# Optimization experiments

Measured on AMD Instinct MI355X. Metric: run time of the kernel, lower is better.

Reference implementation:

```python
import jax, jax.numpy as jnp
import numpy as np
import math

DIM = 384
NUM_HEADS = 12
WS = 8  # window_size


def setup_inputs() -> dict:
    key = jax.random.key(0)
    k1, k2, k3 = jax.random.split(key, 3)
    B, N, C = 16, 4096, DIM
    x = jax.random.normal(k1, (B, N, C), dtype=jnp.float32)
    W_qkv = jax.random.normal(k2, (C, 3 * C), dtype=jnp.float32) * 0.02
    b_qkv = jnp.zeros((3 * C,), dtype=jnp.float32)
    W_proj = jax.random.normal(k3, (C, C), dtype=jnp.float32) * 0.02
    return {"x": x, "W_qkv": W_qkv, "b_qkv": b_qkv, "W_proj": W_proj}


def window_attention(x, W_qkv, b_qkv, W_proj):
    B, N, C = x.shape
    H = W = int(math.isqrt(N))
    nh = NUM_HEADS
    hd = C // nh
    scale = hd ** (-0.5)
    ws = WS
    pad_h = (ws - H % ws) % ws
    pad_w = (ws - W % ws) % ws
    xg = x.reshape(B, H, W, C)
    if pad_h or pad_w:
        xg = jnp.pad(xg, ((0, 0), (0, pad_h), (0, pad_w), (0, 0)))
    Hp, Wp = H + pad_h, W + pad_w
    nH, nW = Hp // ws, Wp // ws
    # partition into windows: [B, nWin, ws*ws, C]
    xw = xg.reshape(B, nH, ws, nW, ws, C).transpose(0, 1, 3, 2, 4, 5)
    xw = xw.reshape(B, nH * nW, ws * ws, C)
    # qkv projection
    qkv = xw @ W_qkv + b_qkv  # [B, nWin, ws2, 3C]
    qkv = qkv.reshape(B, nH * nW, ws * ws, 3, nh, hd)
    q = qkv[..., 0, :, :].transpose(0, 1, 3, 2, 4)  # [B, nWin, nh, ws2, hd]
    k = qkv[..., 1, :, :].transpose(0, 1, 3, 2, 4)
    v = qkv[..., 2, :, :].transpose(0, 1, 3, 2, 4)
    attn = jnp.einsum('bwhqd,bwhkd->bwhqk', q, k) * scale
    attn = jax.nn.softmax(attn, axis=-1)
    out = jnp.einsum('bwhqk,bwhkd->bwhqd', attn, v)
    out = out.transpose(0, 1, 3, 2, 4).reshape(B, nH * nW, ws * ws, C)
    out = out @ W_proj
    # un-partition windows
    out = out.reshape(B, nH, nW, ws, ws, C).transpose(0, 1, 3, 2, 4, 5)
    out = out.reshape(B, Hp, Wp, C)
    if pad_h or pad_w:
        out = out[:, :H, :W, :]
    return out.reshape(B, H * W, C)


def reference(x, W_qkv, b_qkv, W_proj):
    return window_attention(x, W_qkv, b_qkv, W_proj)
```

## Files before the change

### kernel.cpp

```cpp
#include <hip/hip_runtime.h>
#include <hip/hip_bf16.h>


typedef _Float16 f16;
typedef f16 f16x8 __attribute__((ext_vector_type(8)));
typedef f16 f16x4 __attribute__((ext_vector_type(4)));
typedef float f32x4 __attribute__((ext_vector_type(4)));

#define MFMA_F16(a, b, c) __builtin_amdgcn_mfma_f32_16x16x32_f16((a), (b), (c), 0, 0, 0)

#define AS_G __attribute__((address_space(1)))
#define AS_L __attribute__((address_space(3)))
#define GLOAD_LDS16(gp, lp) \
  __builtin_amdgcn_global_load_lds((const AS_G void*)(gp), (AS_L void*)(lp), 16, 0, 0)
#define WAITVM_(N) asm volatile("s_waitcnt vmcnt(" #N ")" ::: "memory")
#define WAITVM(N) WAITVM_(N)

namespace {
constexpr int kC = 384;
constexpr int kNTok = 4096;
constexpr float kScale = 0.17677669529663687f;
constexpr int kWqPackChunks = 72 * 12 * 64;
constexpr int kWpPackChunks = 24 * 12 * 64;
constexpr size_t kWqPackBytes = (size_t)kWqPackChunks * 16;
constexpr size_t kWpPackBytes = (size_t)kWpPackChunks * 16;
constexpr size_t kQkvWsBytes = (size_t)65536 * 1152 * 2;
constexpr size_t kWsNeed = kWqPackBytes + kWpPackBytes + kQkvWsBytes;
constexpr int kPrepXBlocks = 12288;
constexpr int kQkvPackChunksFb = 6 * 12 * 12 * 64;
}


__global__ void prep_all(const float* __restrict__ x,
                         const float* __restrict__ Wqkv,
                         const float* __restrict__ Wproj,
                         f16* __restrict__ xw, f16* __restrict__ wq_pack,
                         f16* __restrict__ wp_pack) {
  int blk = blockIdx.x;
  if (blk < kPrepXBlocks) {
    int c = blk * 256 + threadIdx.x;
    int lane = c & 63;
    int t = c >> 6;
    int ks = t % 12;
    int mb = t / 12;
    int l15 = lane & 15, g = lane >> 4;
    int m = mb * 16 + l15;
    int b = m >> 12;
    int win = (m >> 6) & 63;
    int tok = m & 63;
    int n = ((win >> 3) * 8 + (tok >> 3)) * 64 + (win & 7) * 8 + (tok & 7);
    const float* src = x + ((size_t)(b << 12) + n) * kC + ks * 32 + g * 8;
    float4 v0 = *reinterpret_cast<const float4*>(src);
    float4 v1 = *reinterpret_cast<const float4*>(src + 4);
    f16x8 h = {(f16)v0.x, (f16)v0.y, (f16)v0.z, (f16)v0.w,
               (f16)v1.x, (f16)v1.y, (f16)v1.z, (f16)v1.w};
    *reinterpret_cast<f16x8*>(xw + (size_t)c * 8) = h;
    return;
  }
  int i = (blk - kPrepXBlocks) * 256 + threadIdx.x;
  if (i < kWqPackChunks) {
    int lane = i & 63;
    int chunk = i >> 6;
    int ks = chunk % 12;
    int t = chunk / 12;
    int l15 = lane & 15, g = lane >> 4;
    int n3 = t * 16 + l15;
    int k0 = ks * 32 + g * 8;
    f16x8 v;
    #pragma unroll
    for (int j = 0; j < 8; ++j)
      v[j] = (f16)Wqkv[(size_t)(k0 + j) * (3 * kC) + n3];
    *reinterpret_cast<f16x8*>(wq_pack + (size_t)i * 8) = v;
  } else if (i < kWqPackChunks + kWpPackChunks) {
    int p = i - kWqPackChunks;
    int lane = p & 63;
    int chunk = p >> 6;
    int ks = chunk % 12;
    int t = chunk / 12;
    int l15 = lane & 15, g = lane >> 4;
    int n = t * 16 + l15;
    int k0 = ks * 32 + g * 8;
    f16x8 v;
    #pragma unroll
    for (int j = 0; j < 8; ++j)
      v[j] = (f16)Wproj[(size_t)(k0 + j) * kC + n];
    *reinterpret_cast<f16x8*>(wp_pack + (size_t)p * 8) = v;
  }
}

__global__ __launch_bounds__(512, 4) void qkv_gemm6(
    const f16* __restrict__ xw, const float* __restrict__ b_qkv,
    const f16* __restrict__ wq_pack, f16* __restrict__ qkv_ws) {
  __shared__ alignas(1024) char smem[73728];

  const int tid = threadIdx.x;
  const int wid = tid >> 6;
  const int lane = tid & 63;
  const int g = lane >> 4;
  const int l15 = lane & 15;
  const int wm = wid >> 1;
  const int wn = wid & 1;

  int bid = blockIdx.x;
  int wg = (bid & 7) * 288 + (bid >> 3);
  int m_grp = wg / 9;
  int n_grp = wg - m_grp * 9;
  const int mb0 = m_grp * 16;
  const int nb0 = n_grp * 8;

  #define STAGE(KS, BUF)                                                       \
    do {                                                                       \
      const f16* ga0 =                                                         \
          xw + (((size_t)(mb0 + wid) * 12 + (KS)) * 64 + lane) * 8;            \
      const f16* ga1 =                                                         \
          xw + (((size_t)(mb0 + 8 + wid) * 12 + (KS)) * 64 + lane) * 8;        \
      const f16* gb0 =                                                         \
          wq_pack + (((size_t)(nb0 + wid) * 12 + (KS)) * 64 + lane) * 8;       \
      char* la = smem + (BUF) * 24576 + wid * 1024;                            \
      char* lb = smem + (BUF) * 24576 + 16384 + wid * 1024;                    \
      GLOAD_LDS16(ga0, la);                                                    \
      GLOAD_LDS16(ga1, la + 8192);                                             \
      GLOAD_LDS16(gb0, lb);                                                    \
    } while (0)

  f32x4 acc[4][4];
  #pragma unroll
  for (int mt = 0; mt < 4; ++mt)
    #pragma unroll
    for (int nt = 0; nt < 4; ++nt) acc[mt][nt] = {0.f, 0.f, 0.f, 0.f};

  STAGE(0, 0);
  STAGE(1, 1);
  STAGE(2, 2);
  WAITVM(6);
  __builtin_amdgcn_sched_barrier(0);
  __builtin_amdgcn_s_barrier();

  #define KITER(T, ENDVM)                                                      \
    do {                                                                       \
      constexpr int buf = (T) % 3;                                             \
      f16x8 af[4], bf[4];                                                      \
      _Pragma("unroll") for (int mt = 0; mt < 4; ++mt) af[mt] =                \
          *reinterpret_cast<const f16x8*>(smem + buf * 24576 +                 \
                                          (wm * 4 + mt) * 1024 + lane * 16);   \
      _Pragma("unroll") for (int nt = 0; nt < 4; ++nt) bf[nt] =                \
          *reinterpret_cast<const f16x8*>(smem + buf * 24576 + 16384 +         \
                                          (wn * 4 + nt) * 1024 + lane * 16);   \
      asm volatile("s_waitcnt lgkmcnt(0)" ::: "memory");                       \
      __builtin_amdgcn_sched_barrier(0);                                       \
      __builtin_amdgcn_s_barrier();                                            \
      if ((T) < 9) {                                                           \
        STAGE((T) + 3, buf);                                                   \
      }                                                                        \
      __builtin_amdgcn_s_setprio(1);                                           \
      _Pragma("unroll") for (int mt = 0; mt < 4; ++mt)                         \
          _Pragma("unroll") for (int nt = 0; nt < 4; ++nt) acc[mt][nt] =       \
          MFMA_F16(af[mt], bf[nt], acc[mt][nt]);                               \
      __builtin_amdgcn_s_setprio(0);                                           \
      WAITVM(ENDVM);                                                           \
      __builtin_amdgcn_sched_barrier(0);                                       \
      __builtin_amdgcn_s_barrier();                                            \
    } while (0)

  KITER(0, 6);
  KITER(1, 6);
  KITER(2, 6);
  KITER(3, 6);
  KITER(4, 6);
  KITER(5, 6);
  KITER(6, 6);
  KITER(7, 6);
  KITER(8, 6);
  KITER(9, 3);
  KITER(10, 0);
  KITER(11, 0);
  #undef KITER
  #undef STAGE

  f16* eo = (f16*)smem;
  #pragma unroll
  for (int nt = 0; nt < 4; ++nt) {
    int col128 = wn * 64 + nt * 16 + l15;
    float bias = b_qkv[n_grp * 128 + col128];
    int hsec_loc = wn * 2 + (nt >> 1);
    int d = col128 & 31;
    int sec = (n_grp * 4 + hsec_loc) / 12;
    int base = (wm * 4 + hsec_loc) * 2048;
    #pragma unroll
    for (int mt = 0; mt < 4; ++mt) {
      #pragma unroll
      for (int j = 0; j < 4; ++j) {
        int tok = mt * 16 + g * 4 + j;
        f16 hv = (f16)(acc[mt][nt][j] + bias);
        if (sec == 2)
          eo[base + d * 64 + (tok ^ ((d & 7) << 3))] = hv;
        else
          eo[base + tok * 32 + d] = hv;
      }
    }
  }
  __syncthreads();
  #pragma unroll
  for (int i = 0; i < 8; ++i) {
    int u = tid + i * 512;
    int win_loc = u >> 10;
    int cbl = (u >> 8) & 3;
    int inner = u & 255;
    int cb = n_grp * 4 + cbl;
    int h = cb % 12;
    int sec = cb / 12;
    size_t dst = ((size_t)(m_grp * 4 + win_loc) * 36 + h * 3 + sec) * 2048 +
                 (size_t)inner * 8;
    f16x8 hv;
    if (sec == 2) {
      int d = inner >> 3;
      int t0 = inner & 7;
      hv = *reinterpret_cast<const f16x8*>(eo + (win_loc * 4 + cbl) * 2048 +
                                           d * 64 + ((t0 * 8) ^ ((d & 7) << 3)));
    } else {
      hv = *reinterpret_cast<const f16x8*>(eo + (size_t)u * 8);
    }
    *reinterpret_cast<f16x8*>(qkv_ws + dst) = hv;
  }
}

__device__ __forceinline__ void load_qkv(const f16* __restrict__ hb,
                                         f16x8 (&qf)[4], f16x8 (&kf)[4],
                                         f16x8 (&vf)[2][2], int g, int l15) {
  #pragma unroll
  for (int mt = 0; mt < 4; ++mt)
    qf[mt] = *reinterpret_cast<const f16x8*>(hb + (mt * 16 + l15) * 32 + g * 8);
  #pragma unroll
  for (int nt = 0; nt < 4; ++nt)
    kf[nt] = *reinterpret_cast<const f16x8*>(hb + 2048 + (nt * 16 + l15) * 32 +
                                             g * 8);
  #pragma unroll
  for (int nd = 0; nd < 2; ++nd)
    #pragma unroll
    for (int ks = 0; ks < 2; ++ks)
      vf[nd][ks] = *reinterpret_cast<const f16x8*>(
          hb + 4096 + (nd * 16 + l15) * 64 + ks * 32 + g * 8);
}

__device__ __forceinline__ void attn_one(const f16x8 (&qf)[4],
                                         const f16x8 (&kf)[4],
                                         const f16x8 (&vf)[2][2],
                                         f16 (&ao)[64][392], f16 (&ps)[16][68],
                                         int wid, int g, int l15) {
  const f32x4 zero4 = {0.f, 0.f, 0.f, 0.f};
  #pragma unroll
  for (int mt = 0; mt < 4; ++mt) {
    f32x4 sw0 = MFMA_F16(kf[0], qf[mt], zero4);
    f32x4 sw1 = MFMA_F16(kf[1], qf[mt], zero4);
    f32x4 sw2 = MFMA_F16(kf[2], qf[mt], zero4);
    f32x4 sw3 = MFMA_F16(kf[3], qf[mt], zero4);
    float p[16];
    #pragma unroll
    for (int j = 0; j < 4; ++j) {
      p[j] = sw0[j] * kScale;
      p[4 + j] = sw1[j] * kScale;
      p[8 + j] = sw2[j] * kScale;
      p[12 + j] = sw3[j] * kScale;
    }
    float m0 = fmaxf(fmaxf(p[0], p[1]), fmaxf(p[2], p[3]));
    float m1 = fmaxf(fmaxf(p[4], p[5]), fmaxf(p[6], p[7]));
    float m2 = fmaxf(fmaxf(p[8], p[9]), fmaxf(p[10], p[11]));
    float m3 = fmaxf(fmaxf(p[12], p[13]), fmaxf(p[14], p[15]));
    float mx = fmaxf(fmaxf(m0, m1), fmaxf(m2, m3));
    mx = fmaxf(mx, __shfl_xor(mx, 16));
    mx = fmaxf(mx, __shfl_xor(mx, 32));
    #pragma unroll
    for (int i = 0; i < 16; ++i) p[i] = __expf(p[i] - mx);
    float s01 = (p[0] + p[1]) + (p[2] + p[3]);
    float s23 = (p[4] + p[5]) + (p[6] + p[7]);
    float s45 = (p[8] + p[9]) + (p[10] + p[11]);
    float s67 = (p[12] + p[13]) + (p[14] + p[15]);
    float s = (s01 + s23) + (s45 + s67);
    s += __shfl_xor(s, 16);
    s += __shfl_xor(s, 32);
    float inv = __builtin_amdgcn_rcpf(s);
    #pragma unroll
    for (int nt = 0; nt < 4; ++nt) {
      f16x4 h = {(f16)(p[nt * 4] * inv), (f16)(p[nt * 4 + 1] * inv),
                 (f16)(p[nt * 4 + 2] * inv), (f16)(p[nt * 4 + 3] * inv)};
      *reinterpret_cast<f16x4*>(&ps[l15][nt * 16 + g * 4]) = h;
    }
    f32x4 o0 = zero4, o1 = zero4;
    #pragma unroll
    for (int ks = 0; ks < 2; ++ks) {
      f16x8 pa = *reinterpret_cast<const f16x8*>(&ps[l15][ks * 32 + g * 8]);
      o0 = MFMA_F16(pa, vf[0][ks], o0);
      o1 = MFMA_F16(pa, vf[1][ks], o1);
    }
    #pragma unroll
    for (int j = 0; j < 4; ++j) {
      ao[mt * 16 + g * 4 + j][wid * 32 + l15] = (f16)o0[j];
      ao[mt * 16 + g * 4 + j][wid * 32 + 16 + l15] = (f16)o1[j];
    }
  }
}

__device__ __forceinline__ void proj_store(const f16 (&ao)[64][392],
                                           const f16* __restrict__ wp_pack,
                                           float* __restrict__ out, int b,
                                           int win, int wid, int g, int l15,
                                           int lane) {
  const f32x4 zero4 = {0.f, 0.f, 0.f, 0.f};
  const int wh = win >> 3, ww = win & 7;
  f32x4 pacc[4][2];
  #pragma unroll
  for (int mt = 0; mt < 4; ++mt) {
    pacc[mt][0] = zero4;
    pacc[mt][1] = zero4;
  }
  const f16* pp0 = wp_pack + ((size_t)((wid * 2) * 12) * 64 + lane) * 8;
  const f16* pp1 = wp_pack + ((size_t)((wid * 2 + 1) * 12) * 64 + lane) * 8;
  f16x8 pb0[2], pb1[2];
  pb0[0] = *reinterpret_cast<const f16x8*>(pp0);
  pb1[0] = *reinterpret_cast<const f16x8*>(pp1);
  #pragma unroll
  for (int ks = 0; ks < 12; ++ks) {
    const int cur = ks & 1;
    if (ks < 11) {
      pb0[cur ^ 1] = *reinterpret_cast<const f16x8*>(pp0 + (ks + 1) * 512);
      pb1[cur ^ 1] = *reinterpret_cast<const f16x8*>(pp1 + (ks + 1) * 512);
    }
    f16x8 paf[4];
    #pragma unroll
    for (int mt = 0; mt < 4; ++mt)
      paf[mt] = *reinterpret_cast<const f16x8*>(
          &ao[mt * 16 + l15][ks * 32 + g * 8]);
    #pragma unroll
    for (int mt = 0; mt < 4; ++mt) {
      pacc[mt][0] = MFMA_F16(paf[mt], pb0[cur], pacc[mt][0]);
      pacc[mt][1] = MFMA_F16(paf[mt], pb1[cur], pacc[mt][1]);
    }
  }
  const size_t outbase = (size_t)b * kNTok * kC;
  #pragma unroll
  for (int mt = 0; mt < 4; ++mt) {
    #pragma unroll
    for (int j = 0; j < 4; ++j) {
      int rr = mt * 16 + g * 4 + j;
      int n = (wh * 8 + (rr >> 3)) * 64 + ww * 8 + (rr & 7);
      float* orow = out + outbase + (size_t)n * kC + wid * 32;
      orow[l15] = pacc[mt][0][j];
      orow[16 + l15] = pacc[mt][1][j];
    }
  }
}

__global__ __launch_bounds__(768, 3) void attn_proj3(
    const f16* __restrict__ qkv_ws, const f16* __restrict__ wp_pack,
    float* __restrict__ out) {
  __shared__ alignas(16) f16 ao[64][392];
  __shared__ alignas(16) f16 p_s[12][16][68];

  const int tid = threadIdx.x;
  const int wid = tid >> 6;
  const int lane = tid & 63;
  const int g = lane >> 4;
  const int l15 = lane & 15;

  int bid = (int)blockIdx.x;
  int w2 = (bid & 7) * 64 + (bid >> 3);
  const int b = w2 >> 5;
  const int win0 = (w2 & 31) * 2;
  const int win1 = win0 + 1;

  const f16* hb0 = qkv_ws + ((size_t)(b * 64 + win0) * 36 + wid * 3) * 2048;
  const f16* hb1 = hb0 + 36 * 2048;

  f16x8 qA[4], kA[4], vA[2][2], qB[4], kB[4], vB[2][2];
  load_qkv(hb0, qA, kA, vA, g, l15);
  __builtin_amdgcn_sched_barrier(0);
  attn_one(qA, kA, vA, ao, p_s[wid], wid, g, l15);
  load_qkv(hb1, qB, kB, vB, g, l15);
  __builtin_amdgcn_sched_barrier(0);
  __syncthreads();
  proj_store(ao, wp_pack, out, b, win0, wid, g, l15, lane);
  __syncthreads();
  attn_one(qB, kB, vB, ao, p_s[wid], wid, g, l15);
  __syncthreads();
  proj_store(ao, wp_pack, out, b, win1, wid, g, l15, lane);
}


__global__ void prep_weights_fb(const float* __restrict__ Wqkv,
                                const float* __restrict__ Wproj,
                                f16* __restrict__ wq_pack,
                                f16* __restrict__ wp_pack) {
  int i = blockIdx.x * 256 + threadIdx.x;
  if (i < kQkvPackChunksFb) {
    int lane = i & 63;
    int chunk = i >> 6;
    int ks = chunk % 12;
    int t = (chunk / 12) % 12;
    int hp = chunk / 144;
    int l15 = lane & 15, g = lane >> 4;
    int base = t * 16;
    int hh = base / 96;
    int cc = base - hh * 96;
    int sec = cc >> 5;
    int dbhi = cc & 31;
    int n3 = sec * kC + (2 * hp + hh) * 32 + dbhi + l15;
    int k0 = ks * 32 + g * 8;
    f16x8 v;
    #pragma unroll
    for (int j = 0; j < 8; ++j)
      v[j] = (f16)Wqkv[(size_t)(k0 + j) * (3 * kC) + n3];
    *reinterpret_cast<f16x8*>(wq_pack + (size_t)i * 8) = v;
  } else if (i < kQkvPackChunksFb + kWpPackChunks) {
    int p = i - kQkvPackChunksFb;
    int lane = p & 63;
    int chunk = p >> 6;
    int ks = chunk % 12;
    int t = chunk / 12;
    int l15 = lane & 15, g = lane >> 4;
    int n = t * 16 + l15;
    int k0 = ks * 32 + g * 8;
    f16x8 v;
    #pragma unroll
    for (int j = 0; j < 8; ++j)
      v[j] = (f16)Wproj[(size_t)(k0 + j) * kC + n];
    *reinterpret_cast<f16x8*>(wp_pack + (size_t)p * 8) = v;
  }
}

__global__ __launch_bounds__(512, 2) void win_attn_fused_fb(
    const float* __restrict__ x, const float* __restrict__ b_qkv,
    const f16* __restrict__ wq_pack, const f16* __restrict__ wp_pack,
    float* __restrict__ out) {
  __shared__ alignas(16) f16 xs[64][392];
  __shared__ alignas(16) f16 ao[64][392];
  __shared__ alignas(16) f16 q_s[2][64][40];
  __shared__ alignas(16) f16 k_s[2][64][40];
  __shared__ alignas(16) f16 vT[2][32][72];
  __shared__ alignas(16) f16 p_s[8][16][72];

  const int tid = threadIdx.x;
  const int wid = tid >> 6;
  const int lane = tid & 63;
  const int g = lane >> 4;
  const int l15 = lane & 15;
  const int wm = wid >> 2;
  const int wn = wid & 3;

  const int blk = blockIdx.x;
  const int b = blk >> 6;
  const int win = blk & 63;
  const int wh = win >> 3;
  const int ww = win & 7;

  const f32x4 zero4 = {0.f, 0.f, 0.f, 0.f};

  {
    const float* xb = x + (size_t)b * kNTok * kC;
    #pragma unroll
    for (int it = 0; it < 12; ++it) {
      int idx = tid + it * 512;
      int r = idx / 96;
      int c4 = idx - r * 96;
      int n = (wh * 8 + (r >> 3)) * 64 + ww * 8 + (r & 7);
      float4 v = *reinterpret_cast<const float4*>(xb + (size_t)n * kC + c4 * 4);
      f16x4 hv = {(f16)v.x, (f16)v.y, (f16)v.z, (f16)v.w};
      *reinterpret_cast<f16x4*>(&xs[r][c4 * 4]) = hv;
    }
  }
  __syncthreads();

  for (int hp = 0; hp < 6; ++hp) {
    f32x4 acc[2][3];
    #pragma unroll
    for (int mt = 0; mt < 2; ++mt)
      #pragma unroll
      for (int nt = 0; nt < 3; ++nt) acc[mt][nt] = zero4;

    const f16* bptr[3];
    int secv[3], dbv[3], hhv[3];
    #pragma unroll
    for (int nt = 0; nt < 3; ++nt) {
      int t = wn * 3 + nt;
      int base = t * 16;
      int hh = base / 96;
      int cc = base - hh * 96;
      hhv[nt] = hh;
      secv[nt] = cc >> 5;
      dbv[nt] = cc & 31;
      bptr[nt] = wq_pack + ((size_t)((hp * 12 + t) * 12) * 64 + lane) * 8;
    }

    f16x8 bf[4][3];
    f16x8 af[2][2];
    #pragma unroll
    for (int p = 0; p < 3; ++p)
      #pragma unroll
      for (int nt = 0; nt < 3; ++nt)
        bf[p][nt] = *reinterpret_cast<const f16x8*>(bptr[nt] + p * 512);
    #pragma unroll
    for (int mt = 0; mt < 2; ++mt)
      af[0][mt] = *reinterpret_cast<const f16x8*>(
          &xs[wm * 32 + mt * 16 + l15][g * 8]);

    #pragma unroll
    for (int ks = 0; ks < 12; ++ks) {
      const int cur = ks & 3;
      const int ca = ks & 1;
      if (ks < 9) {
        const int nx = (ks + 3) & 3;
        #pragma unroll
        for (int nt = 0; nt < 3; ++nt)
          bf[nx][nt] =
              *reinterpret_cast<const f16x8*>(bptr[nt] + (ks + 3) * 512);
      }
      if (ks < 11) {
        #pragma unroll
        for (int mt = 0; mt < 2; ++mt)
          af[ca ^ 1][mt] = *reinterpret_cast<const f16x8*>(
              &xs[wm * 32 + mt * 16 + l15][(ks + 1) * 32 + g * 8]);
      }
      #pragma unroll
      for (int mt = 0; mt < 2; ++mt)
        #pragma unroll
        for (int nt = 0; nt < 3; ++nt)
          acc[mt][nt] = MFMA_F16(af[ca][mt], bf[cur][nt], acc[mt][nt]);
    }

    #pragma unroll
    for (int nt = 0; nt < 3; ++nt) {
      int hh = hhv[nt], sec = secv[nt];
      int col = dbv[nt] + l15;
      float bias = b_qkv[sec * kC + (2 * hp + hh) * 32 + col];
      #pragma unroll
      for (int mt = 0; mt < 2; ++mt) {
        #pragma unroll
        for (int j = 0; j < 4; ++j) {
          int r = wm * 32 + mt * 16 + g * 4 + j;
          f16 hv = (f16)(acc[mt][nt][j] + bias);
          if (sec == 0) q_s[hh][r][col] = hv;
          else if (sec == 1) k_s[hh][r][col] = hv;
          else vT[hh][col][r] = hv;
        }
      }
    }
    __syncthreads();

    f32x4 sacc[4];
    #pragma unroll
    for (int nt = 0; nt < 4; ++nt) sacc[nt] = zero4;
    f16x8 qa = *reinterpret_cast<const f16x8*>(&q_s[wm][wn * 16 + l15][g * 8]);
    #pragma unroll
    for (int nt = 0; nt < 4; ++nt) {
      f16x8 kb =
          *reinterpret_cast<const f16x8*>(&k_s[wm][nt * 16 + l15][g * 8]);
      sacc[nt] = MFMA_F16(qa, kb, sacc[nt]);
    }

    float pv[4][4];
    #pragma unroll
    for (int j = 0; j < 4; ++j) {
      float m = -1e30f;
      #pragma unroll
      for (int nt = 0; nt < 4; ++nt) {
        pv[nt][j] = sacc[nt][j] * kScale;
        m = fmaxf(m, pv[nt][j]);
      }
      m = fmaxf(m, __shfl_xor(m, 1));
      m = fmaxf(m, __shfl_xor(m, 2));
      m = fmaxf(m, __shfl_xor(m, 4));
      m = fmaxf(m, __shfl_xor(m, 8));
      float s = 0.f;
      #pragma unroll
      for (int nt = 0; nt < 4; ++nt) {
        pv[nt][j] = __expf(pv[nt][j] - m);
        s += pv[nt][j];
      }
      s += __shfl_xor(s, 1);
      s += __shfl_xor(s, 2);
      s += __shfl_xor(s, 4);
      s += __shfl_xor(s, 8);
      float inv = 1.0f / s;
      #pragma unroll
      for (int nt = 0; nt < 4; ++nt)
        p_s[wid][g * 4 + j][nt * 16 + l15] = (f16)(pv[nt][j] * inv);
    }

    f32x4 oacc[2];
    oacc[0] = zero4;
    oacc[1] = zero4;
    #pragma unroll
    for (int ks = 0; ks < 2; ++ks) {
      f16x8 pa =
          *reinterpret_cast<const f16x8*>(&p_s[wid][l15][ks * 32 + g * 8]);
      #pragma unroll
      for (int nt = 0; nt < 2; ++nt) {
        f16x8 vb = *reinterpret_cast<const f16x8*>(
            &vT[wm][nt * 16 + l15][ks * 32 + g * 8]);
        oacc[nt] = MFMA_F16(pa, vb, oacc[nt]);
      }
    }
    #pragma unroll
    for (int nt = 0; nt < 2; ++nt)
      #pragma unroll
      for (int j = 0; j < 4; ++j)
        ao[wn * 16 + g * 4 + j][(2 * hp + wm) * 32 + nt * 16 + l15] =
            (f16)oacc[nt][j];
    __syncthreads();
  }

  f32x4 pacc[2][6];
  #pragma unroll
  for (int mt = 0; mt < 2; ++mt)
    #pragma unroll
    for (int nt = 0; nt < 6; ++nt) pacc[mt][nt] = zero4;

  const f16* pptr[6];
  #pragma unroll
  for (int nt = 0; nt < 6; ++nt) {
    int t = wn * 6 + nt;
    pptr[nt] = wp_pack + ((size_t)(t * 12) * 64 + lane) * 8;
  }
  f16x8 pbf[3][6];
  f16x8 paf[2][2];
  #pragma unroll
  for (int p = 0; p < 2; ++p)
    #pragma unroll
    for (int nt = 0; nt < 6; ++nt)
      pbf[p][nt] = *reinterpret_cast<const f16x8*>(pptr[nt] + p * 512);
  #pragma unroll
  for (int mt = 0; mt < 2; ++mt)
    paf[0][mt] =
        *reinterpret_cast<const f16x8*>(&ao[wm * 32 + mt * 16 + l15][g * 8]);

  #pragma unroll
  for (int ks = 0; ks < 12; ++ks) {
    const int cur = ks % 3;
    const int ca = ks & 1;
    if (ks < 10) {
      const int nx = (ks + 2) % 3;
      #pragma unroll
      for (int nt = 0; nt < 6; ++nt)
        pbf[nx][nt] =
            *reinterpret_cast<const f16x8*>(pptr[nt] + (ks + 2) * 512);
    }
    if (ks < 11) {
      #pragma unroll
      for (int mt = 0; mt < 2; ++mt)
        paf[ca ^ 1][mt] = *reinterpret_cast<const f16x8*>(
            &ao[wm * 32 + mt * 16 + l15][(ks + 1) * 32 + g * 8]);
    }
    #pragma unroll
    for (int mt = 0; mt < 2; ++mt)
      #pragma unroll
      for (int nt = 0; nt < 6; ++nt)
        pacc[mt][nt] = MFMA_F16(paf[ca][mt], pbf[cur][nt], pacc[mt][nt]);
  }

  const size_t outbase = (size_t)b * kNTok * kC;
  #pragma unroll
  for (int mt = 0; mt < 2; ++mt) {
    #pragma unroll
    for (int j = 0; j < 4; ++j) {
      int r = wm * 32 + mt * 16 + g * 4 + j;
      int n = (wh * 8 + (r >> 3)) * 64 + ww * 8 + (r & 7);
      float* orow = out + outbase + (size_t)n * kC + wn * 96;
      #pragma unroll
      for (int nt = 0; nt < 6; ++nt) orow[nt * 16 + l15] = pacc[mt][nt][j];
    }
  }
}


extern "C" void kernel_launch(void* const* d_in, const int* in_sizes, int n_in,
                              void* d_out, int out_size, void* d_ws,
                              size_t ws_size, hipStream_t stream) {
  const float* x = (const float*)d_in[0];
  const float* Wqkv = (const float*)d_in[1];
  const float* bqkv = (const float*)d_in[2];
  const float* Wproj = (const float*)d_in[3];
  float* out = (float*)d_out;

  if (ws_size >= kWsNeed) {
    f16* wq_pack = (f16*)d_ws;
    f16* wp_pack = (f16*)((char*)d_ws + kWqPackBytes);
    f16* qkv_ws = (f16*)((char*)d_ws + kWqPackBytes + kWpPackBytes);
    f16* xw = (f16*)d_out;

    int prep_blocks =
        kPrepXBlocks + (kWqPackChunks + kWpPackChunks + 255) / 256;
    hipLaunchKernelGGL(prep_all, dim3(prep_blocks), dim3(256), 0, stream, x,
                       Wqkv, Wproj, xw, wq_pack, wp_pack);
    hipLaunchKernelGGL(qkv_gemm6, dim3(2304), dim3(512), 0, stream, xw, bqkv,
                       wq_pack, qkv_ws);
    hipLaunchKernelGGL(attn_proj3, dim3(512), dim3(768), 0, stream, qkv_ws,
                       wp_pack, out);
  } else {
    f16* wq_pack = (f16*)d_ws;
    f16* wp_pack = (f16*)((char*)d_ws + (size_t)kQkvPackChunksFb * 16);
    int prep_threads = kQkvPackChunksFb + kWpPackChunks;
    hipLaunchKernelGGL(prep_weights_fb, dim3((prep_threads + 255) / 256),
                       dim3(256), 0, stream, Wqkv, Wproj, wq_pack, wp_pack);
    hipLaunchKernelGGL(win_attn_fused_fb, dim3(16 * 64), dim3(512), 0, stream,
                       x, bqkv, wq_pack, wp_pack, out);
  }
}
```

Measured before the change: 160.8 us.

## Use four larger-tile warps per block in QKV GEMM instead of eight

Cuts the QKV GEMM block from 8 to 4 wavefronts while keeping the same 256x128 output tile. Each wave now computes a 64x128 sub-tile (4x8 MFMA tiles) and reuses the A fragments across twice as many B fragments, which lowers LDS reads per MFMA. Each thread issues 6 async global-to-LDS loads per stage, and the vmcnt waits are scaled to match. The trade-off is more accumulator registers per thread and fewer waves per block available to hide latency.

```diff
diff --git a/kernel.cpp b/kernel.cpp
--- a/kernel.cpp
+++ b/kernel.cpp
@@ -88,7 +88,7 @@
   }
 }
 
-__global__ __launch_bounds__(512, 4) void qkv_gemm6(
+__global__ __launch_bounds__(256, 2) void qkv_gemm8(
     const f16* __restrict__ xw, const float* __restrict__ b_qkv,
     const f16* __restrict__ wq_pack, f16* __restrict__ qkv_ws) {
   __shared__ alignas(1024) char smem[73728];
@@ -98,8 +98,6 @@
   const int lane = tid & 63;
   const int g = lane >> 4;
   const int l15 = lane & 15;
-  const int wm = wid >> 1;
-  const int wn = wid & 1;
 
   int bid = blockIdx.x;
   int wg = (bid & 7) * 288 + (bid >> 3);
@@ -110,42 +108,43 @@
 
   #define STAGE(KS, BUF)                                                       \
     do {                                                                       \
-      const f16* ga0 =                                                         \
-          xw + (((size_t)(mb0 + wid) * 12 + (KS)) * 64 + lane) * 8;            \
-      const f16* ga1 =                                                         \
-          xw + (((size_t)(mb0 + 8 + wid) * 12 + (KS)) * 64 + lane) * 8;        \
-      const f16* gb0 =                                                         \
-          wq_pack + (((size_t)(nb0 + wid) * 12 + (KS)) * 64 + lane) * 8;       \
-      char* la = smem + (BUF) * 24576 + wid * 1024;                            \
-      char* lb = smem + (BUF) * 24576 + 16384 + wid * 1024;                    \
-      GLOAD_LDS16(ga0, la);                                                    \
-      GLOAD_LDS16(ga1, la + 8192);                                             \
-      GLOAD_LDS16(gb0, lb);                                                    \
+      char* la = smem + (BUF) * 24576;                                         \
+      char* lb = la + 16384;                                                   \
+      _Pragma("unroll") for (int q = 0; q < 4; ++q) {                          \
+        const f16* ga =                                                        \
+            xw + (((size_t)(mb0 + wid + q * 4) * 12 + (KS)) * 64 + lane) * 8;  \
+        GLOAD_LDS16(ga, la + (wid + q * 4) * 1024);                            \
+      }                                                                        \
+      _Pragma("unroll") for (int q = 0; q < 2; ++q) {                          \
+        const f16* gb = wq_pack +                                              \
+            (((size_t)(nb0 + wid + q * 4) * 12 + (KS)) * 64 + lane) * 8;       \
+        GLOAD_LDS16(gb, lb + (wid + q * 4) * 1024);                            \
+      }                                                                        \
     } while (0)
 
-  f32x4 acc[4][4];
+  f32x4 acc[4][8];
   #pragma unroll
   for (int mt = 0; mt < 4; ++mt)
     #pragma unroll
-    for (int nt = 0; nt < 4; ++nt) acc[mt][nt] = {0.f, 0.f, 0.f, 0.f};
+    for (int nt = 0; nt < 8; ++nt) acc[mt][nt] = {0.f, 0.f, 0.f, 0.f};
 
   STAGE(0, 0);
   STAGE(1, 1);
   STAGE(2, 2);
-  WAITVM(6);
+  WAITVM(12);
   __builtin_amdgcn_sched_barrier(0);
   __builtin_amdgcn_s_barrier();
 
   #define KITER(T, ENDVM)                                                      \
     do {                                                                       \
       constexpr int buf = (T) % 3;                                             \
-      f16x8 af[4], bf[4];                                                      \
+      f16x8 af[4], bf[8];                                                      \
       _Pragma("unroll") for (int mt = 0; mt < 4; ++mt) af[mt] =                \
           *reinterpret_cast<const f16x8*>(smem + buf * 24576 +                 \
-                                          (wm * 4 + mt) * 1024 + lane * 16);   \
-      _Pragma("unroll") for (int nt = 0; nt < 4; ++nt) bf[nt] =                \
+                                          (wid * 4 + mt) * 1024 + lane * 16);  \
+      _Pragma("unroll") for (int nt = 0; nt < 8; ++nt) bf[nt] =                \
           *reinterpret_cast<const f16x8*>(smem + buf * 24576 + 16384 +         \
-                                          (wn * 4 + nt) * 1024 + lane * 16);   \
+                                          nt * 1024 + lane * 16);              \
       asm volatile("s_waitcnt lgkmcnt(0)" ::: "memory");                       \
       __builtin_amdgcn_sched_barrier(0);                                       \
       __builtin_amdgcn_s_barrier();                                            \
@@ -154,7 +153,7 @@
       }                                                                        \
       __builtin_amdgcn_s_setprio(1);                                           \
       _Pragma("unroll") for (int mt = 0; mt < 4; ++mt)                         \
-          _Pragma("unroll") for (int nt = 0; nt < 4; ++nt) acc[mt][nt] =       \
+          _Pragma("unroll") for (int nt = 0; nt < 8; ++nt) acc[mt][nt] =       \
           MFMA_F16(af[mt], bf[nt], acc[mt][nt]);                               \
       __builtin_amdgcn_s_setprio(0);                                           \
       WAITVM(ENDVM);                                                           \
@@ -162,16 +161,16 @@
       __builtin_amdgcn_s_barrier();                                            \
     } while (0)
 
-  KITER(0, 6);
-  KITER(1, 6);
-  KITER(2, 6);
-  KITER(3, 6);
-  KITER(4, 6);
-  KITER(5, 6);
-  KITER(6, 6);
-  KITER(7, 6);
-  KITER(8, 6);
-  KITER(9, 3);
+  KITER(0, 12);
+  KITER(1, 12);
+  KITER(2, 12);
+  KITER(3, 12);
+  KITER(4, 12);
+  KITER(5, 12);
+  KITER(6, 12);
+  KITER(7, 12);
+  KITER(8, 12);
+  KITER(9, 6);
   KITER(10, 0);
   KITER(11, 0);
   #undef KITER
@@ -179,13 +178,13 @@
 
   f16* eo = (f16*)smem;
   #pragma unroll
-  for (int nt = 0; nt < 4; ++nt) {
-    int col128 = wn * 64 + nt * 16 + l15;
+  for (int nt = 0; nt < 8; ++nt) {
+    int col128 = nt * 16 + l15;
     float bias = b_qkv[n_grp * 128 + col128];
-    int hsec_loc = wn * 2 + (nt >> 1);
+    int hsec_loc = nt >> 1;
     int d = col128 & 31;
     int sec = (n_grp * 4 + hsec_loc) / 12;
-    int base = (wm * 4 + hsec_loc) * 2048;
+    int base = (wid * 4 + hsec_loc) * 2048;
     #pragma unroll
     for (int mt = 0; mt < 4; ++mt) {
       #pragma unroll
@@ -201,8 +200,8 @@
   }
   __syncthreads();
   #pragma unroll
-  for (int i = 0; i < 8; ++i) {
-    int u = tid + i * 512;
+  for (int i = 0; i < 16; ++i) {
+    int u = tid + i * 256;
     int win_loc = u >> 10;
     int cbl = (u >> 8) & 3;
     int inner = u & 255;
@@ -690,7 +689,7 @@
         kPrepXBlocks + (kWqPackChunks + kWpPackChunks + 255) / 256;
     hipLaunchKernelGGL(prep_all, dim3(prep_blocks), dim3(256), 0, stream, x,
                        Wqkv, Wproj, xw, wq_pack, wp_pack);
-    hipLaunchKernelGGL(qkv_gemm6, dim3(2304), dim3(512), 0, stream, xw, bqkv,
+    hipLaunchKernelGGL(qkv_gemm8, dim3(2304), dim3(256), 0, stream, xw, bqkv,
                        wq_pack, qkv_ws);
     hipLaunchKernelGGL(attn_proj3, dim3(512), dim3(768), 0, stream, qkv_ws,
                        wp_pack, out);
```

New measurement: 172.1 us. 7.0% more time.
